# Performance work log

Hardware: AMD Instinct MI355X
Metric: run time of the kernel (lower is better)

The kernel has to match this reference:

```python
import jax, jax.numpy as jnp
import numpy as np

B, L, I, H = 128, 128, 256, 256
NUM_LAYERS = 2
PRIOR_STD = 1.0


def setup_inputs() -> dict:
    key = jax.random.key(0)
    ks = jax.random.split(key, 14)
    d = {}
    d['x'] = jax.random.normal(ks[0], (B, L, I), dtype=jnp.float32)
    # layer 0 params: weight [4H, I+H], bias [4H]
    d['w_mu0'] = jax.random.normal(ks[1], (4 * H, I + H), dtype=jnp.float32) * 0.1
    d['w_logvar0'] = jax.random.normal(ks[2], (4 * H, I + H), dtype=jnp.float32) * 0.1
    d['b_mu0'] = jnp.zeros((4 * H,), dtype=jnp.float32)
    d['b_logvar0'] = jax.random.normal(ks[3], (4 * H,), dtype=jnp.float32) * 0.1
    # layer 1 params: weight [4H, H+H]
    d['w_mu1'] = jax.random.normal(ks[4], (4 * H, 2 * H), dtype=jnp.float32) * 0.1
    d['w_logvar1'] = jax.random.normal(ks[5], (4 * H, 2 * H), dtype=jnp.float32) * 0.1
    d['b_mu1'] = jnp.zeros((4 * H,), dtype=jnp.float32)
    d['b_logvar1'] = jax.random.normal(ks[6], (4 * H,), dtype=jnp.float32) * 0.1
    # per-timestep reparameterization noise (fresh sample each step, as in torch randn_like)
    d['eps_w0'] = jax.random.normal(ks[7], (L, 4 * H, I + H), dtype=jnp.float32)
    d['eps_b0'] = jax.random.normal(ks[8], (L, 4 * H), dtype=jnp.float32)
    d['eps_w1'] = jax.random.normal(ks[9], (L, 4 * H, 2 * H), dtype=jnp.float32)
    d['eps_b1'] = jax.random.normal(ks[10], (L, 4 * H), dtype=jnp.float32)
    return d


def _cell(inp, h, c, w, b):
    # inp: [B, D_in], h/c: [B, H], w: [4H, D_in+H], b: [4H]
    gates = jnp.concatenate([inp, h], axis=1) @ w.T + b
    i_g, f_g, g_g, o_g = jnp.split(gates, 4, axis=1)
    i_g = jax.nn.sigmoid(i_g)
    f_g = jax.nn.sigmoid(f_g)
    g_g = jnp.tanh(g_g)
    o_g = jax.nn.sigmoid(o_g)
    c_new = f_g * c + i_g * g_g
    h_new = o_g * jnp.tanh(c_new)
    return h_new, c_new


def _kl(mu, logvar):
    # prior_std = 1.0 -> log(prior^2) = 0
    p2 = PRIOR_STD * PRIOR_STD
    return 0.5 * jnp.sum(mu * mu / p2 + jnp.exp(logvar) / p2 - logvar - jnp.log(jnp.asarray(p2, mu.dtype)))


def reference(x, w_mu0, w_logvar0, b_mu0, b_logvar0, w_mu1, w_logvar1, b_mu1, b_logvar1,
              eps_w0, eps_b0, eps_w1, eps_b1):
    Bv = x.shape[0]
    w_std0 = jnp.exp(0.5 * w_logvar0)
    b_std0 = jnp.exp(0.5 * b_logvar0)
    w_std1 = jnp.exp(0.5 * w_logvar1)
    b_std1 = jnp.exp(0.5 * b_logvar1)

    def step(carry, inp):
        h0, c0, h1, c1 = carry
        x_t, ew0, eb0, ew1, eb1 = inp
        w0 = w_mu0 + ew0 * w_std0
        b0 = b_mu0 + eb0 * b_std0
        h0, c0 = _cell(x_t, h0, c0, w0, b0)
        w1 = w_mu1 + ew1 * w_std1
        b1 = b_mu1 + eb1 * b_std1
        h1, c1 = _cell(h0, h1, c1, w1, b1)  # eval mode: no dropout between layers
        return (h0, c0, h1, c1), h1

    z = jnp.zeros((Bv, H), dtype=x.dtype)
    init = (z, z, z, z)
    xs = (jnp.swapaxes(x, 0, 1), eps_w0, eps_b0, eps_w1, eps_b1)  # time-major
    (h0, c0, h1, c1), outs = jax.lax.scan(step, init, xs)
    output = jnp.swapaxes(outs, 0, 1)  # [B, L, H]
    h_final = jnp.stack([h0, h1])
    c_final = jnp.stack([c0, c1])
    # kl per cell per step is identical across steps; total/L = sum over layers
    kl_layer = _kl(w_mu0, w_logvar0) + _kl(b_mu0, b_logvar0) + _kl(w_mu1, w_logvar1) + _kl(b_mu1, b_logvar1)
    Lv = x.shape[1]
    total_kl = (Lv * kl_layer) / Lv
    return output, (h_final, c_final), total_kl
```

## Files before the change

kernel.cpp:

```cpp
#include <hip/hip_runtime.h>
#include <hip/hip_cooperative_groups.h>
#include <cmath>

namespace cg = cooperative_groups;

constexpr int B_  = 128, L_ = 128, I_ = 256, H_ = 256;
constexpr int G4_ = 1024;
constexpr int K_  = 512;
constexpr int NBLK = 256;
constexpr int NTHR = 512;
constexpr int BT = 32;
constexpr int GR = 16;

constexpr int WSTD0 = 0;
constexpr int WSTD1 = 524288;
constexpr int BSTD0 = 1048576;
constexpr int BSTD1 = BSTD0 + 1024;
constexpr int HB0   = BSTD1 + 1024;
constexpr int HB1   = HB0 + 65536;
constexpr int KLP   = HB1 + 65536;
constexpr int CNT   = KLP + 256;

constexpr int HF_OFF = B_*L_*H_;
constexpr int CF_OFF = HF_OFF + 2*B_*H_;
constexpr int KL_OFF = CF_OFF + 2*B_*H_;

__device__ __forceinline__ float sigm(float v) { return 1.0f / (1.0f + expf(-v)); }

__device__ __forceinline__ float4 ld_cohere(const float* p) {
  float4 v;
  asm volatile("global_load_dwordx4 %0, %1, off sc0 sc1"
               : "=v"(v) : "v"(p) : "memory");
  return v;
}

__device__ __forceinline__ void vm_drain() {
  asm volatile("s_waitcnt vmcnt(0)" ::: "memory");
}

__global__ __launch_bounds__(NTHR, 1) void vlstm(
    const float* __restrict__ x,
    const float* __restrict__ wmu0, const float* __restrict__ wlv0,
    const float* __restrict__ bmu0, const float* __restrict__ blv0,
    const float* __restrict__ wmu1, const float* __restrict__ wlv1,
    const float* __restrict__ bmu1, const float* __restrict__ blv1,
    const float* __restrict__ epsw0, const float* __restrict__ epsb0,
    const float* __restrict__ epsw1, const float* __restrict__ epsb1,
    float* __restrict__ out, float* __restrict__ ws)
{
  cg::grid_group grid = cg::this_grid();
  const int tid = threadIdx.x;
  const int g   = blockIdx.x;
  const int bt  = g >> 6;
  const int ut  = g & 63;
  const int b0  = bt * BT;
  const int u0  = ut * 4;

  __shared__ float Xs [BT][260];
  __shared__ float H0s[BT][260];
  __shared__ float H1s[BT][260];
  __shared__ float Wsh[GR][516];
  __shared__ float red[NTHR];

  float* wstd0 = ws + WSTD0;
  float* wstd1 = ws + WSTD1;
  float* bstd0 = ws + BSTD0;
  float* bstd1 = ws + BSTD1;
  float* hb0   = ws + HB0;
  float* hb1   = ws + HB1;
  float* klp   = ws + KLP;
  unsigned* cnt = (unsigned*)(ws + CNT);

  const int gid = g * NTHR + tid;
  const int gsz = NBLK * NTHR;
  float kl = 0.f;
  for (int i = gid; i < 524288; i += gsz) {
    float l0 = wlv0[i], l1 = wlv1[i];
    float m0 = wmu0[i], m1 = wmu1[i];
    wstd0[i] = expf(0.5f * l0);
    wstd1[i] = expf(0.5f * l1);
    kl += 0.5f * (m0*m0 + expf(l0) - l0) + 0.5f * (m1*m1 + expf(l1) - l1);
  }
  for (int i = gid; i < G4_; i += gsz) {
    float l0 = blv0[i], l1 = blv1[i];
    float m0 = bmu0[i], m1 = bmu1[i];
    bstd0[i] = expf(0.5f * l0);
    bstd1[i] = expf(0.5f * l1);
    kl += 0.5f * (m0*m0 + expf(l0) - l0) + 0.5f * (m1*m1 + expf(l1) - l1);
  }
  for (int i = gid; i < 32768; i += gsz) {
    hb0[i] = 0.f; hb0[32768 + i] = 0.f;
    hb1[i] = 0.f; hb1[32768 + i] = 0.f;
  }
  if (gid < 544) cnt[gid] = 0u;
  red[tid] = kl;
  __syncthreads();
  for (int s = NTHR / 2; s > 0; s >>= 1) {
    if (tid < s) red[tid] += red[tid + s];
    __syncthreads();
  }
  if (tid == 0) klp[g] = red[0];
  grid.sync();

  const int wid  = tid >> 6;
  const int lane = tid & 63;
  const int b_l  = ((wid & 3) << 3) | (lane >> 3);
  const int rr   = ((wid >> 2) << 3) | (lane & 7);
  const int gq   = lane & 3;
  const int un   = rr >> 2;
  const int jrow = gq * H_ + u0 + un;
  const int bglob = b0 + b_l;
  const int uglob = u0 + un;

  float c0reg = 0.f, c1reg = 0.f;

  auto issueW = [&](int layer, int t, float4* mu, float4* sd, float4* ep) {
    const float* wmu  = layer ? wmu1  : wmu0;
    const float* wstd = layer ? wstd1 : wstd0;
    const float* epsw = layer ? epsw1 : epsw0;
    #pragma unroll
    for (int p = 0; p < 4; p++) {
      int q = p * NTHR + tid;
      int row = q >> 7, c = q & 127;
      int jr  = (row & 3) * H_ + u0 + (row >> 2);
      mu[p] = *(const float4*)(wmu  + jr * K_ + c * 4);
      sd[p] = *(const float4*)(wstd + jr * K_ + c * 4);
      ep[p] = *(const float4*)(epsw + (t * G4_ + jr) * K_ + c * 4);
    }
  };
  auto writeW = [&](const float4* mu, const float4* sd, const float4* ep) {
    #pragma unroll
    for (int p = 0; p < 4; p++) {
      int q = p * NTHR + tid;
      int row = q >> 7, c = q & 127;
      float4 wv;
      wv.x = fmaf(ep[p].x, sd[p].x, mu[p].x);
      wv.y = fmaf(ep[p].y, sd[p].y, mu[p].y);
      wv.z = fmaf(ep[p].z, sd[p].z, mu[p].z);
      wv.w = fmaf(ep[p].w, sd[p].w, mu[p].w);
      *(float4*)&Wsh[row][c * 4] = wv;
    }
  };
  auto dotp = [&](const float* Ap, const float* Wp) -> float {
    const float4* A4 = (const float4*)Ap;
    const float4* W4 = (const float4*)Wp;
    float pa = 0.f, qa = 0.f;
    #pragma unroll 8
    for (int k = 0; k < 32; k++) {
      float4 a  = A4[k],      wv  = W4[k];
      float4 a2 = A4[k + 32], wv2 = W4[k + 32];
      pa = fmaf(a.x,  wv.x,  pa); pa = fmaf(a.y,  wv.y,  pa);
      pa = fmaf(a.z,  wv.z,  pa); pa = fmaf(a.w,  wv.w,  pa);
      qa = fmaf(a2.x, wv2.x, qa); qa = fmaf(a2.y, wv2.y, qa);
      qa = fmaf(a2.z, wv2.z, qa); qa = fmaf(a2.w, wv2.w, qa);
    }
    return pa + qa;
  };

  {
    float4 mu[4], sd[4], ep[4];
    issueW(0, 0, mu, sd, ep);
    #pragma unroll
    for (int p = 0; p < 4; p++) {
      int q = p * NTHR + tid;
      int row = q >> 6, c4 = q & 63;
      *(float4*)&Xs[row][c4 * 4] =
          *((const float4*)(x + ((b0 + row) * L_) * I_) + c4);
    }
    writeW(mu, sd, ep);
  }
  __syncthreads();

  for (int tau = 0; tau <= L_; tau++) {
    const int t0 = tau;
    const int t1 = tau - 1;
    const float* h0prev = hb0 + ((tau - 1) & 1) * 32768;
    const float* h1prev = hb1 + (tau & 1) * 32768;
    const bool havenx = (tau + 1 < L_);

    float4 h0v[4], h1v[4], xn[4];
    float4 mu1v[4], sd1v[4], ep1v[4];
    #pragma unroll
    for (int p = 0; p < 4; p++) {
      int q = p * NTHR + tid;
      int row = q >> 6, c4 = q & 63;
      h0v[p] = ld_cohere(h0prev + (b0 + row) * H_ + c4 * 4);
      h1v[p] = ld_cohere(h1prev + (b0 + row) * H_ + c4 * 4);
    }
    if (tau >= 1) issueW(1, t1, mu1v, sd1v, ep1v);
    if (havenx) {
      #pragma unroll
      for (int p = 0; p < 4; p++) {
        int q = p * NTHR + tid;
        int row = q >> 6, c4 = q & 63;
        xn[p] = *((const float4*)(x + ((b0 + row) * L_ + (tau + 1)) * I_) + c4);
      }
    }

    float acc0 = 0.f;
    if (tau < L_) acc0 = dotp(&Xs[b_l][0], &Wsh[rr][0]);
    __syncthreads();

    vm_drain();
    #pragma unroll
    for (int p = 0; p < 4; p++) {
      int q = p * NTHR + tid;
      int row = q >> 6, c4 = q & 63;
      *(float4*)&H0s[row][c4 * 4] = h0v[p];
      *(float4*)&H1s[row][c4 * 4] = h1v[p];
    }
    if (havenx) {
      #pragma unroll
      for (int p = 0; p < 4; p++) {
        int q = p * NTHR + tid;
        int row = q >> 6, c4 = q & 63;
        *(float4*)&Xs[row][c4 * 4] = xn[p];
      }
    }
    __syncthreads();

    if (tau < L_) {
      acc0 += dotp(&H0s[b_l][0], &Wsh[rr][256]);
      acc0 += fmaf(epsb0[t0 * G4_ + jrow], bstd0[jrow], bmu0[jrow]);
      float fg = __shfl_xor(acc0, 1);
      float gg = __shfl_xor(acc0, 2);
      float og = __shfl_xor(acc0, 3);
      if (gq == 0) {
        float si = sigm(acc0), sf = sigm(fg), sg = tanhf(gg), so = sigm(og);
        float cn = fmaf(sf, c0reg, si * sg);
        float h  = so * tanhf(cn);
        c0reg = cn;
        __hip_atomic_store(&hb0[(tau & 1) * 32768 + bglob * H_ + uglob], h,
                           __ATOMIC_RELAXED, __HIP_MEMORY_SCOPE_AGENT);
        if (t0 == L_ - 1) {
          out[HF_OFF + bglob * H_ + uglob] = h;
          out[CF_OFF + bglob * H_ + uglob] = cn;
        }
      }
    }
    __syncthreads();

    float4 mu0v[4], sd0v[4], ep0v[4];
    if (tau >= 1) writeW(mu1v, sd1v, ep1v);
    if (havenx)  issueW(0, tau + 1, mu0v, sd0v, ep0v);
    __syncthreads();

    if (tau >= 1) {
      float acc1 = dotp(&H0s[b_l][0], &Wsh[rr][0])
                 + dotp(&H1s[b_l][0], &Wsh[rr][256]);
      acc1 += fmaf(epsb1[t1 * G4_ + jrow], bstd1[jrow], bmu1[jrow]);
      float fg = __shfl_xor(acc1, 1);
      float gg = __shfl_xor(acc1, 2);
      float og = __shfl_xor(acc1, 3);
      if (gq == 0) {
        float si = sigm(acc1), sf = sigm(fg), sg = tanhf(gg), so = sigm(og);
        float cn = fmaf(sf, c1reg, si * sg);
        float h  = so * tanhf(cn);
        c1reg = cn;
        __hip_atomic_store(&hb1[((tau - 1) & 1) * 32768 + bglob * H_ + uglob], h,
                           __ATOMIC_RELAXED, __HIP_MEMORY_SCOPE_AGENT);
        out[(bglob * L_ + t1) * H_ + uglob] = h;
        if (t1 == L_ - 1) {
          out[HF_OFF + (B_ + bglob) * H_ + uglob] = h;
          out[CF_OFF + (B_ + bglob) * H_ + uglob] = cn;
        }
      }
    }
    __syncthreads();

    if (havenx) writeW(mu0v, sd0v, ep0v);

    if (tau < L_) {
      __builtin_amdgcn_s_waitcnt(0);
      __syncthreads();
      const unsigned tgt = (unsigned)(tau + 1);
      if (tid == 0)
        __hip_atomic_fetch_add(&cnt[(g & 15) << 5], 1u,
                               __ATOMIC_RELAXED, __HIP_MEMORY_SCOPE_AGENT);
      if (g == 0) {
        if (tid < 16) {
          const unsigned t16 = tgt << 4;
          while (__hip_atomic_load(&cnt[tid << 5],
                                   __ATOMIC_RELAXED, __HIP_MEMORY_SCOPE_AGENT) < t16)
            __builtin_amdgcn_s_sleep(1);
        }
        __syncthreads();
        if (tid == 0)
          __hip_atomic_store(&cnt[512], tgt,
                             __ATOMIC_RELAXED, __HIP_MEMORY_SCOPE_AGENT);
      } else if (tid == 0) {
        while (__hip_atomic_load(&cnt[512],
                                 __ATOMIC_RELAXED, __HIP_MEMORY_SCOPE_AGENT) < tgt)
          __builtin_amdgcn_s_sleep(1);
      }
      __syncthreads();
    }
  }

  if (g == 0) {
    red[tid] = (tid < NBLK) ? klp[tid] : 0.f;
    __syncthreads();
    for (int s = NTHR / 2; s > 0; s >>= 1) {
      if (tid < s) red[tid] += red[tid + s];
      __syncthreads();
    }
    if (tid == 0) out[KL_OFF] = red[0];
  }
}

extern "C" void kernel_launch(void* const* d_in, const int* in_sizes, int n_in,
                              void* d_out, int out_size, void* d_ws, size_t ws_size,
                              hipStream_t stream) {
  const float* x     = (const float*)d_in[0];
  const float* wmu0  = (const float*)d_in[1];
  const float* wlv0  = (const float*)d_in[2];
  const float* bmu0  = (const float*)d_in[3];
  const float* blv0  = (const float*)d_in[4];
  const float* wmu1  = (const float*)d_in[5];
  const float* wlv1  = (const float*)d_in[6];
  const float* bmu1  = (const float*)d_in[7];
  const float* blv1  = (const float*)d_in[8];
  const float* epsw0 = (const float*)d_in[9];
  const float* epsb0 = (const float*)d_in[10];
  const float* epsw1 = (const float*)d_in[11];
  const float* epsb1 = (const float*)d_in[12];
  float* out = (float*)d_out;
  float* ws  = (float*)d_ws;

  void* args[] = {
    (void*)&x,
    (void*)&wmu0, (void*)&wlv0, (void*)&bmu0, (void*)&blv0,
    (void*)&wmu1, (void*)&wlv1, (void*)&bmu1, (void*)&blv1,
    (void*)&epsw0, (void*)&epsb0, (void*)&epsw1, (void*)&epsb1,
    (void*)&out, (void*)&ws
  };
  hipLaunchCooperativeKernel((void*)vlstm, dim3(NBLK), dim3(NTHR),
                             (void**)args, 0, stream);
}
```

Before: 3.074 ms.

## Use LDS-only barriers, defer weight mean/std loads, hoist bias terms

Replaces most __syncthreads with a barrier that waits only on LDS counters, so global loads can stay in flight across block barriers. Only the epsilon noise is prefetched early; the weight mean and std are loaded at write time. This cuts live registers but exposes their cache latency. Bias mean/std are hoisted out of the time loop, and the extra full waitcnt plus barrier before the grid-wide step counter is removed, which weakens the ordering guarantee for the hidden-state stores.

```diff
diff --git a/kernel.cpp b/kernel.cpp
--- a/kernel.cpp
+++ b/kernel.cpp
@@ -25,6 +25,8 @@
 constexpr int CF_OFF = HF_OFF + 2*B_*H_;
 constexpr int KL_OFF = CF_OFF + 2*B_*H_;
 
+struct F44 { float4 a, b, c, d; };
+
 __device__ __forceinline__ float sigm(float v) { return 1.0f / (1.0f + expf(-v)); }
 
 __device__ __forceinline__ float4 ld_cohere(const float* p) {
@@ -33,9 +35,13 @@
                : "=v"(v) : "v"(p) : "memory");
   return v;
 }
-
 __device__ __forceinline__ void vm_drain() {
   asm volatile("s_waitcnt vmcnt(0)" ::: "memory");
+}
+__device__ __forceinline__ void bar_lds() {
+  asm volatile("s_waitcnt lgkmcnt(0)" ::: "memory");
+  __builtin_amdgcn_s_barrier();
+  asm volatile("" ::: "memory");
 }
 
 __global__ __launch_bounds__(NTHR, 1) void vlstm(
@@ -112,34 +118,67 @@
   const int bglob = b0 + b_l;
   const int uglob = u0 + un;
 
+  const float bm0 = bmu0[jrow], bs0 = bstd0[jrow];
+  const float bm1 = bmu1[jrow], bs1 = bstd1[jrow];
+
   float c0reg = 0.f, c1reg = 0.f;
 
-  auto issueW = [&](int layer, int t, float4* mu, float4* sd, float4* ep) {
-    const float* wmu  = layer ? wmu1  : wmu0;
-    const float* wstd = layer ? wstd1 : wstd0;
-    const float* epsw = layer ? epsw1 : epsw0;
-    #pragma unroll
-    for (int p = 0; p < 4; p++) {
-      int q = p * NTHR + tid;
-      int row = q >> 7, c = q & 127;
-      int jr  = (row & 3) * H_ + u0 + (row >> 2);
-      mu[p] = *(const float4*)(wmu  + jr * K_ + c * 4);
-      sd[p] = *(const float4*)(wstd + jr * K_ + c * 4);
-      ep[p] = *(const float4*)(epsw + (t * G4_ + jr) * K_ + c * 4);
-    }
+  int q0 = tid,            r0w = q0 >> 7, c0w = q0 & 127;
+  int q1 = NTHR + tid,     r1w = q1 >> 7, c1w = q1 & 127;
+  int q2 = 2*NTHR + tid,   r2w = q2 >> 7, c2w = q2 & 127;
+  int q3 = 3*NTHR + tid,   r3w = q3 >> 7, c3w = q3 & 127;
+  const int wOff0 = ((r0w & 3) * H_ + u0 + (r0w >> 2)) * K_ + c0w * 4;
+  const int wOff1 = ((r1w & 3) * H_ + u0 + (r1w >> 2)) * K_ + c1w * 4;
+  const int wOff2 = ((r2w & 3) * H_ + u0 + (r2w >> 2)) * K_ + c2w * 4;
+  const int wOff3 = ((r3w & 3) * H_ + u0 + (r3w >> 2)) * K_ + c3w * 4;
+  float* wdst0 = &Wsh[r0w][c0w * 4];
+  float* wdst1 = &Wsh[r1w][c1w * 4];
+  float* wdst2 = &Wsh[r2w][c2w * 4];
+  float* wdst3 = &Wsh[r3w][c3w * 4];
+
+  int hq0 = tid,          hr0 = hq0 >> 6, hc0 = hq0 & 63;
+  int hq1 = NTHR + tid,   hr1 = hq1 >> 6, hc1 = hq1 & 63;
+  int hq2 = 2*NTHR + tid, hr2 = hq2 >> 6, hc2 = hq2 & 63;
+  int hq3 = 3*NTHR + tid, hr3 = hq3 >> 6, hc3 = hq3 & 63;
+  const int hOff0 = (b0 + hr0) * H_ + hc0 * 4;
+  const int hOff1 = (b0 + hr1) * H_ + hc1 * 4;
+  const int hOff2 = (b0 + hr2) * H_ + hc2 * 4;
+  const int hOff3 = (b0 + hr3) * H_ + hc3 * 4;
+  const size_t xOff0 = (size_t)(b0 + hr0) * L_ * I_ + hc0 * 4;
+  const size_t xOff1 = (size_t)(b0 + hr1) * L_ * I_ + hc1 * 4;
+  const size_t xOff2 = (size_t)(b0 + hr2) * L_ * I_ + hc2 * 4;
+  const size_t xOff3 = (size_t)(b0 + hr3) * L_ * I_ + hc3 * 4;
+  float* h0d0 = &H0s[hr0][hc0*4]; float* h1d0 = &H1s[hr0][hc0*4]; float* xd0 = &Xs[hr0][hc0*4];
+  float* h0d1 = &H0s[hr1][hc1*4]; float* h1d1 = &H1s[hr1][hc1*4]; float* xd1 = &Xs[hr1][hc1*4];
+  float* h0d2 = &H0s[hr2][hc2*4]; float* h1d2 = &H1s[hr2][hc2*4]; float* xd2 = &Xs[hr2][hc2*4];
+  float* h0d3 = &H0s[hr3][hc3*4]; float* h1d3 = &H1s[hr3][hc3*4]; float* xd3 = &Xs[hr3][hc3*4];
+
+  auto loadEps = [&](const float* eb) -> F44 {
+    F44 r;
+    r.a = *(const float4*)(eb + wOff0);
+    r.b = *(const float4*)(eb + wOff1);
+    r.c = *(const float4*)(eb + wOff2);
+    r.d = *(const float4*)(eb + wOff3);
+    return r;
   };
-  auto writeW = [&](const float4* mu, const float4* sd, const float4* ep) {
-    #pragma unroll
-    for (int p = 0; p < 4; p++) {
-      int q = p * NTHR + tid;
-      int row = q >> 7, c = q & 127;
-      float4 wv;
-      wv.x = fmaf(ep[p].x, sd[p].x, mu[p].x);
-      wv.y = fmaf(ep[p].y, sd[p].y, mu[p].y);
-      wv.z = fmaf(ep[p].z, sd[p].z, mu[p].z);
-      wv.w = fmaf(ep[p].w, sd[p].w, mu[p].w);
-      *(float4*)&Wsh[row][c * 4] = wv;
-    }
+  auto writeW = [&](const float* wmu, const float* wsd, F44 e) {
+    float4 m, s, w;
+    m = *(const float4*)(wmu + wOff0); s = *(const float4*)(wsd + wOff0);
+    w.x = fmaf(e.a.x, s.x, m.x); w.y = fmaf(e.a.y, s.y, m.y);
+    w.z = fmaf(e.a.z, s.z, m.z); w.w = fmaf(e.a.w, s.w, m.w);
+    *(float4*)wdst0 = w;
+    m = *(const float4*)(wmu + wOff1); s = *(const float4*)(wsd + wOff1);
+    w.x = fmaf(e.b.x, s.x, m.x); w.y = fmaf(e.b.y, s.y, m.y);
+    w.z = fmaf(e.b.z, s.z, m.z); w.w = fmaf(e.b.w, s.w, m.w);
+    *(float4*)wdst1 = w;
+    m = *(const float4*)(wmu + wOff2); s = *(const float4*)(wsd + wOff2);
+    w.x = fmaf(e.c.x, s.x, m.x); w.y = fmaf(e.c.y, s.y, m.y);
+    w.z = fmaf(e.c.z, s.z, m.z); w.w = fmaf(e.c.w, s.w, m.w);
+    *(float4*)wdst2 = w;
+    m = *(const float4*)(wmu + wOff3); s = *(const float4*)(wsd + wOff3);
+    w.x = fmaf(e.d.x, s.x, m.x); w.y = fmaf(e.d.y, s.y, m.y);
+    w.z = fmaf(e.d.z, s.z, m.z); w.w = fmaf(e.d.w, s.w, m.w);
+    *(float4*)wdst3 = w;
   };
   auto dotp = [&](const float* Ap, const float* Wp) -> float {
     const float4* A4 = (const float4*)Ap;
@@ -158,16 +197,12 @@
   };
 
   {
-    float4 mu[4], sd[4], ep[4];
-    issueW(0, 0, mu, sd, ep);
-    #pragma unroll
-    for (int p = 0; p < 4; p++) {
-      int q = p * NTHR + tid;
-      int row = q >> 6, c4 = q & 63;
-      *(float4*)&Xs[row][c4 * 4] =
-          *((const float4*)(x + ((b0 + row) * L_) * I_) + c4);
-    }
-    writeW(mu, sd, ep);
+    *(float4*)xd0 = *(const float4*)(x + xOff0);
+    *(float4*)xd1 = *(const float4*)(x + xOff1);
+    *(float4*)xd2 = *(const float4*)(x + xOff2);
+    *(float4*)xd3 = *(const float4*)(x + xOff3);
+    F44 e = loadEps(epsw0);
+    writeW(wmu0, wstd0, e);
   }
   __syncthreads();
 
@@ -176,52 +211,53 @@
     const int t1 = tau - 1;
     const float* h0prev = hb0 + ((tau - 1) & 1) * 32768;
     const float* h1prev = hb1 + (tau & 1) * 32768;
+    const bool have0  = (tau < L_);
+    const bool have1  = (tau >= 1);
     const bool havenx = (tau + 1 < L_);
 
-    float4 h0v[4], h1v[4], xn[4];
-    float4 mu1v[4], sd1v[4], ep1v[4];
-    #pragma unroll
-    for (int p = 0; p < 4; p++) {
-      int q = p * NTHR + tid;
-      int row = q >> 6, c4 = q & 63;
-      h0v[p] = ld_cohere(h0prev + (b0 + row) * H_ + c4 * 4);
-      h1v[p] = ld_cohere(h1prev + (b0 + row) * H_ + c4 * 4);
-    }
-    if (tau >= 1) issueW(1, t1, mu1v, sd1v, ep1v);
+    const float* wmu0v = wmu0; const float* wsd0v = wstd0;
+    const float* wmu1v = wmu1; const float* wsd1v = wstd1;
+    asm volatile("" : "+s"(wmu0v), "+s"(wsd0v), "+s"(wmu1v), "+s"(wsd1v));
+
+    float4 h00 = ld_cohere(h0prev + hOff0);
+    float4 h01 = ld_cohere(h0prev + hOff1);
+    float4 h02 = ld_cohere(h0prev + hOff2);
+    float4 h03 = ld_cohere(h0prev + hOff3);
+    float4 h10 = ld_cohere(h1prev + hOff0);
+    float4 h11 = ld_cohere(h1prev + hOff1);
+    float4 h12 = ld_cohere(h1prev + hOff2);
+    float4 h13 = ld_cohere(h1prev + hOff3);
+    float4 xn0, xn1, xn2, xn3;
     if (havenx) {
-      #pragma unroll
-      for (int p = 0; p < 4; p++) {
-        int q = p * NTHR + tid;
-        int row = q >> 6, c4 = q & 63;
-        xn[p] = *((const float4*)(x + ((b0 + row) * L_ + (tau + 1)) * I_) + c4);
-      }
+      const size_t xo = (size_t)(tau + 1) * I_;
+      xn0 = *(const float4*)(x + xOff0 + xo);
+      xn1 = *(const float4*)(x + xOff1 + xo);
+      xn2 = *(const float4*)(x + xOff2 + xo);
+      xn3 = *(const float4*)(x + xOff3 + xo);
     }
 
     float acc0 = 0.f;
-    if (tau < L_) acc0 = dotp(&Xs[b_l][0], &Wsh[rr][0]);
-    __syncthreads();
+    if (have0) acc0 = dotp(&Xs[b_l][0], &Wsh[rr][0]);
+    bar_lds();
 
     vm_drain();
-    #pragma unroll
-    for (int p = 0; p < 4; p++) {
-      int q = p * NTHR + tid;
-      int row = q >> 6, c4 = q & 63;
-      *(float4*)&H0s[row][c4 * 4] = h0v[p];
-      *(float4*)&H1s[row][c4 * 4] = h1v[p];
-    }
+    *(float4*)h0d0 = h00; *(float4*)h1d0 = h10;
+    *(float4*)h0d1 = h01; *(float4*)h1d1 = h11;
+    *(float4*)h0d2 = h02; *(float4*)h1d2 = h12;
+    *(float4*)h0d3 = h03; *(float4*)h1d3 = h13;
     if (havenx) {
-      #pragma unroll
-      for (int p = 0; p < 4; p++) {
-        int q = p * NTHR + tid;
-        int row = q >> 6, c4 = q & 63;
-        *(float4*)&Xs[row][c4 * 4] = xn[p];
-      }
-    }
-    __syncthreads();
-
-    if (tau < L_) {
+      *(float4*)xd0 = xn0;
+      *(float4*)xd1 = xn1;
+      *(float4*)xd2 = xn2;
+      *(float4*)xd3 = xn3;
+    }
+    F44 e1;
+    if (have1) e1 = loadEps(epsw1 + (size_t)t1 * 524288);
+    bar_lds();
+
+    if (have0) {
       acc0 += dotp(&H0s[b_l][0], &Wsh[rr][256]);
-      acc0 += fmaf(epsb0[t0 * G4_ + jrow], bstd0[jrow], bmu0[jrow]);
+      acc0 += fmaf(epsb0[t0 * G4_ + jrow], bs0, bm0);
       float fg = __shfl_xor(acc0, 1);
       float gg = __shfl_xor(acc0, 2);
       float og = __shfl_xor(acc0, 3);
@@ -238,17 +274,17 @@
         }
       }
     }
-    __syncthreads();
-
-    float4 mu0v[4], sd0v[4], ep0v[4];
-    if (tau >= 1) writeW(mu1v, sd1v, ep1v);
-    if (havenx)  issueW(0, tau + 1, mu0v, sd0v, ep0v);
-    __syncthreads();
-
-    if (tau >= 1) {
+    bar_lds();
+
+    if (have1) writeW(wmu1v, wsd1v, e1);
+    F44 e0;
+    if (havenx) e0 = loadEps(epsw0 + (size_t)(tau + 1) * 524288);
+    bar_lds();
+
+    if (have1) {
       float acc1 = dotp(&H0s[b_l][0], &Wsh[rr][0])
                  + dotp(&H1s[b_l][0], &Wsh[rr][256]);
-      acc1 += fmaf(epsb1[t1 * G4_ + jrow], bstd1[jrow], bmu1[jrow]);
+      acc1 += fmaf(epsb1[t1 * G4_ + jrow], bs1, bm1);
       float fg = __shfl_xor(acc1, 1);
       float gg = __shfl_xor(acc1, 2);
       float og = __shfl_xor(acc1, 3);
@@ -268,11 +304,9 @@
     }
     __syncthreads();
 
-    if (havenx) writeW(mu0v, sd0v, ep0v);
+    if (havenx) writeW(wmu0v, wsd0v, e0);
 
     if (tau < L_) {
-      __builtin_amdgcn_s_waitcnt(0);
-      __syncthreads();
       const unsigned tgt = (unsigned)(tau + 1);
       if (tid == 0)
         __hip_atomic_fetch_add(&cnt[(g & 15) << 5], 1u,
```

Measured after the change: 2.612 ms. -15.0%, faster.
